# Optimization experiments

Hardware: AMD Instinct MI355X
Metric: run time of the kernel (lower is better)

## Reference

```python
import jax, jax.numpy as jnp
import numpy as np

TEMPERATURE = 0.07
N, D, NUM_CLASSES = 8192, 1024, 128


def setup_inputs() -> dict:
    key = jax.random.key(0)
    k1, k2 = jax.random.split(key)
    embeddings = jax.random.normal(k1, (N, D), dtype=jnp.float32)
    labels = jax.random.randint(k2, (N,), 0, NUM_CLASSES, dtype=jnp.int64)
    return {"embeddings": embeddings, "labels": labels}


def reference(embeddings, labels):
    # L2-normalize rows (eps matches F.normalize default clamp of 1e-12 on the norm)
    norm = jnp.maximum(jnp.linalg.norm(embeddings, axis=-1, keepdims=True), 1e-12)
    emb = embeddings / norm
    # [N, N] similarity scaled by temperature
    sim = jnp.matmul(emb, emb.T) / TEMPERATURE
    # positive mask: same label, diagonal zeroed
    pos_mask = (labels[:, None] == labels[None, :]).astype(sim.dtype)
    pos_mask = pos_mask * (1.0 - jnp.eye(sim.shape[0], dtype=sim.dtype))
    exp_sim = jnp.exp(sim)
    sum_exp = exp_sim.sum(axis=1)              # [N]
    pos_sum = (exp_sim * pos_mask).sum(axis=1)  # [N]
    loss = -jnp.log(pos_sum / sum_exp)
    return loss.mean()
```

## Files before the change

kernel.cpp:

```cpp
#include <hip/hip_runtime.h>
#include <hip/hip_bf16.h>
#include <math.h>

#define N 8192
#define D 1024
#define BM 256
#define BK 64
#define NTIL 32
#define NBLK 528
#define ITERS 8

typedef __bf16 bf16_t;
typedef bf16_t bf16x4 __attribute__((ext_vector_type(4)));
typedef bf16_t bf16x8 __attribute__((ext_vector_type(8)));
typedef float f32x4 __attribute__((ext_vector_type(4)));

__global__ __launch_bounds__(256) void norm_cast(const float* __restrict__ in,
                                                 bf16_t* __restrict__ out,
                                                 float* __restrict__ sumExp,
                                                 float* __restrict__ posSum) {
    const int wave = threadIdx.x >> 6, lane = threadIdx.x & 63;
    const int row  = blockIdx.x * 4 + wave;
    const float4* src = (const float4*)(in + (size_t)row * D);
    float4 v[4];
    float ss = 0.f;
    #pragma unroll
    for (int i = 0; i < 4; ++i) {
        v[i] = src[lane + 64 * i];
        ss += v[i].x * v[i].x + v[i].y * v[i].y + v[i].z * v[i].z + v[i].w * v[i].w;
    }
    #pragma unroll
    for (int off = 32; off >= 1; off >>= 1) ss += __shfl_xor(ss, off, 64);
    const float scale = 1.0f / fmaxf(sqrtf(ss), 1e-12f);
    bf16x4* dst = (bf16x4*)(out + (size_t)row * D);
    #pragma unroll
    for (int i = 0; i < 4; ++i) {
        bf16x4 o;
        o[0] = (bf16_t)(v[i].x * scale);
        o[1] = (bf16_t)(v[i].y * scale);
        o[2] = (bf16_t)(v[i].z * scale);
        o[3] = (bf16_t)(v[i].w * scale);
        dst[lane + 64 * i] = o;
    }
    if (lane == 0) { sumExp[row] = 0.f; posSum[row] = 0.f; }
}

__global__ __launch_bounds__(512, 2) void gemm_fused(const bf16_t* __restrict__ E,
                                                     const int* __restrict__ labels,
                                                     float* __restrict__ sumExp,
                                                     float* __restrict__ posSum) {
    __shared__ bf16_t As[2][2][128 * 64];
    __shared__ bf16_t Bs[2][2][128 * 64];

    const int b0 = blockIdx.x;
    const int b  = (b0 & 7) * (NBLK / 8) + (b0 >> 3);

    int ti = (int)((sqrtf(8.0f * (float)b + 1.0f) - 1.0f) * 0.5f);
    while ((ti + 1) * (ti + 2) / 2 <= b) ++ti;
    while (ti * (ti + 1) / 2 > b) --ti;
    const int tj = b - ti * (ti + 1) / 2;
    const bool isDiag = (ti == tj);

    const int tid  = threadIdx.x;
    const int wave = tid >> 6;
    const int lane = tid & 63;
    const int lr   = lane & 15;
    const int q    = lane >> 4;
    const int wm   = wave >> 2;
    const int wn   = wave & 3;
    const int rowStart = ti * BM;
    const int colStart = tj * BM;

    f32x4 acc[8][4];
    #pragma unroll
    for (int m = 0; m < 8; ++m)
        #pragma unroll
        for (int n = 0; n < 4; ++n) acc[m][n] = {0.f, 0.f, 0.f, 0.f};

    const int r0  = tid >> 3;
    const int lu0 = tid & 7;
    const char* gA = (const char*)(E + (size_t)rowStart * D) + (size_t)r0 * (D * 2) + lu0 * 16;
    const char* gB = (const char*)(E + (size_t)colStart * D) + (size_t)r0 * (D * 2) + lu0 * 16;

    #define STAGE_A(buf, h, kb) do {                                                     \
        const char* g0_ = gA + (size_t)(h) * (128 * 2048) + (kb);                        \
        char* l0_ = (char*)&As[buf][h][0] + wave * 1024;                                 \
        __builtin_amdgcn_global_load_lds((const __attribute__((address_space(1))) void*)g0_, \
            (__attribute__((address_space(3))) void*)l0_, 16, 0, 0);                     \
        __builtin_amdgcn_global_load_lds(                                                \
            (const __attribute__((address_space(1))) void*)(g0_ + 64 * 2048),            \
            (__attribute__((address_space(3))) void*)(l0_ + 8192), 16, 0, 0);            \
    } while (0)
    #define STAGE_B(buf, h, kb) do {                                                     \
        const char* g0_ = gB + (size_t)(h) * (128 * 2048) + (kb);                        \
        char* l0_ = (char*)&Bs[buf][h][0] + wave * 1024;                                 \
        __builtin_amdgcn_global_load_lds((const __attribute__((address_space(1))) void*)g0_, \
            (__attribute__((address_space(3))) void*)l0_, 16, 0, 0);                     \
        __builtin_amdgcn_global_load_lds(                                                \
            (const __attribute__((address_space(1))) void*)(g0_ + 64 * 2048),            \
            (__attribute__((address_space(3))) void*)(l0_ + 8192), 16, 0, 0);            \
    } while (0)

    const int su0 = (0 + q) * 16;
    const int su1 = (4 + q) * 16;
    const char* rA0 = (const char*)&As[0][wm][0] + lr * 128;
    const char* rA1 = (const char*)&As[1][wm][0] + lr * 128;
    const char* rB0 = (const char*)&Bs[0][wn >> 1][0] + (wn & 1) * 8192 + lr * 128;
    const char* rB1 = (const char*)&Bs[1][wn >> 1][0] + (wn & 1) * 8192 + lr * 128;

    #define LD_A4(DST, RBASE, MOFFB, SU) do {                                            \
        _Pragma("unroll")                                                                \
        for (int m_ = 0; m_ < 4; ++m_)                                                   \
            DST[m_] = *(const bf16x8*)((RBASE) + (MOFFB) + m_ * 2048 + (SU));            \
    } while (0)
    #define LD_B4(DST, RBASE, SU) do {                                                   \
        _Pragma("unroll")                                                                \
        for (int n_ = 0; n_ < 4; ++n_)                                                   \
            DST[n_] = *(const bf16x8*)((RBASE) + n_ * 2048 + (SU));                      \
    } while (0)
    #define MFMA_QUAD(AF, BF, MO) do {                                                   \
        _Pragma("unroll")                                                                \
        for (int m_ = 0; m_ < 4; ++m_) {                                                 \
            _Pragma("unroll")                                                            \
            for (int n_ = 0; n_ < 4; ++n_)                                               \
                acc[(MO) + m_][n_] = __builtin_amdgcn_mfma_f32_16x16x32_bf16(            \
                    AF[m_], BF[n_], acc[(MO) + m_][n_], 0, 0, 0);                        \
        }                                                                                \
    } while (0)
    #define PHASE_MID() do {                                                             \
        __builtin_amdgcn_s_barrier();                                                    \
        asm volatile("s_waitcnt lgkmcnt(0)");                                            \
        __builtin_amdgcn_sched_barrier(0);                                               \
        __builtin_amdgcn_s_setprio(1);                                                   \
    } while (0)
    #define PHASE_END() do {                                                             \
        __builtin_amdgcn_s_setprio(0);                                                   \
        __builtin_amdgcn_s_barrier();                                                    \
    } while (0)

    bf16x8 a0[4], a1[4], bq0[4], bq1[4];

    STAGE_B(0, 0, 0);  STAGE_B(0, 1, 0);
    STAGE_A(0, 0, 0);  STAGE_A(0, 1, 0);
    STAGE_B(1, 0, 128); STAGE_B(1, 1, 128);
    asm volatile("s_waitcnt vmcnt(4)" ::: "memory");
    __builtin_amdgcn_sched_barrier(0);
    __builtin_amdgcn_s_barrier();

    #pragma unroll 1
    for (int it = 0; it < ITERS; ++it) {
        const bool lastIt = (it == ITERS - 1);
        const int kb1 = (2 * it + 1) * 128;
        const int kb2 = (2 * it + 2) * 128;
        const int kb3 = (2 * it + 3) * 128;

        LD_A4(a0, rA0, 0, su0);
        LD_B4(bq0, rB0, su0);
        STAGE_A(1, 0, kb1);
        PHASE_MID();
        MFMA_QUAD(a0, bq0, 0);
        PHASE_END();

        LD_A4(a1, rA0, 0, su1);
        LD_B4(bq1, rB0, su1);
        STAGE_A(1, 1, kb1);
        PHASE_MID();
        MFMA_QUAD(a1, bq1, 0);
        PHASE_END();

        LD_A4(a0, rA0, 8192, su0);
        if (!lastIt) STAGE_B(0, 0, kb2);
        PHASE_MID();
        MFMA_QUAD(a0, bq0, 4);
        PHASE_END();

        LD_A4(a1, rA0, 8192, su1);
        if (!lastIt) {
            STAGE_B(0, 1, kb2);
            asm volatile("s_waitcnt vmcnt(4)" ::: "memory");
        } else {
            asm volatile("s_waitcnt vmcnt(0)" ::: "memory");
        }
        __builtin_amdgcn_sched_barrier(0);
        PHASE_MID();
        MFMA_QUAD(a1, bq1, 4);
        PHASE_END();

        LD_A4(a0, rA1, 0, su0);
        LD_B4(bq0, rB1, su0);
        if (!lastIt) STAGE_A(0, 0, kb2);
        PHASE_MID();
        MFMA_QUAD(a0, bq0, 0);
        PHASE_END();

        LD_A4(a1, rA1, 0, su1);
        LD_B4(bq1, rB1, su1);
        if (!lastIt) STAGE_A(0, 1, kb2);
        PHASE_MID();
        MFMA_QUAD(a1, bq1, 0);
        PHASE_END();

        LD_A4(a0, rA1, 8192, su0);
        if (!lastIt) STAGE_B(1, 0, kb3);
        PHASE_MID();
        MFMA_QUAD(a0, bq0, 4);
        PHASE_END();

        LD_A4(a1, rA1, 8192, su1);
        if (!lastIt) {
            STAGE_B(1, 1, kb3);
            asm volatile("s_waitcnt vmcnt(4)" ::: "memory");
            __builtin_amdgcn_sched_barrier(0);
        }
        PHASE_MID();
        MFMA_QUAD(a1, bq1, 4);
        PHASE_END();
    }

    const float invT = 1.0f / 0.07f;
    int lc[4];
    #pragma unroll
    for (int n = 0; n < 4; ++n)
        lc[n] = labels[colStart + wn * 64 + n * 16 + lr];

    float colAll[4] = {0.f, 0.f, 0.f, 0.f};
    float colPos[4] = {0.f, 0.f, 0.f, 0.f};
    #pragma unroll
    for (int m = 0; m < 8; ++m) {
        #pragma unroll
        for (int e = 0; e < 4; ++e) {
            const int rloc = wm * 128 + m * 16 + q * 4 + e;
            const int gi   = rowStart + rloc;
            const int li   = labels[gi];
            float s_all = 0.f, s_pos = 0.f;
            #pragma unroll
            for (int n = 0; n < 4; ++n) {
                const int cloc = wn * 64 + n * 16 + lr;
                const int gj   = colStart + cloc;
                const float v  = __expf(acc[m][n][e] * invT);
                const bool same = (lc[n] == li);
                s_all += v;
                if (same && gi != gj) s_pos += v;
                if (!isDiag) {
                    colAll[n] += v;
                    if (same) colPos[n] += v;
                }
            }
            #pragma unroll
            for (int off = 1; off < 16; off <<= 1) {
                s_all += __shfl_xor(s_all, off, 64);
                s_pos += __shfl_xor(s_pos, off, 64);
            }
            if (lr == 0) {
                atomicAdd(&sumExp[gi], s_all);
                atomicAdd(&posSum[gi], s_pos);
            }
        }
    }
    if (!isDiag) {
        #pragma unroll
        for (int n = 0; n < 4; ++n) {
            float a = colAll[n], p = colPos[n];
            a += __shfl_xor(a, 16, 64);  a += __shfl_xor(a, 32, 64);
            p += __shfl_xor(p, 16, 64);  p += __shfl_xor(p, 32, 64);
            if (q == 0) {
                const int gj = colStart + wn * 64 + n * 16 + lr;
                atomicAdd(&sumExp[gj], a);
                atomicAdd(&posSum[gj], p);
            }
        }
    }
}

__global__ __launch_bounds__(1024) void finalize(const float* __restrict__ sumExp,
                                                 const float* __restrict__ posSum,
                                                 float* __restrict__ out) {
    const int tid = threadIdx.x;
    float s = 0.f;
    #pragma unroll
    for (int i = tid; i < N; i += 1024)
        s += __logf(sumExp[i] / posSum[i]);
    #pragma unroll
    for (int off = 32; off >= 1; off >>= 1) s += __shfl_xor(s, off, 64);
    __shared__ float red[16];
    if ((tid & 63) == 0) red[tid >> 6] = s;
    __syncthreads();
    if (tid == 0) {
        float t = 0.f;
        #pragma unroll
        for (int i = 0; i < 16; ++i) t += red[i];
        out[0] = t / (float)N;
    }
}

extern "C" void kernel_launch(void* const* d_in, const int* in_sizes, int n_in,
                              void* d_out, int out_size, void* d_ws, size_t ws_size,
                              hipStream_t stream) {
    const float* emb    = (const float*)d_in[0];
    const int*   labels = (const int*)d_in[1];
    float* out = (float*)d_out;

    float*  sumExp = (float*)d_ws;
    float*  posSum = sumExp + N;
    bf16_t* EN     = (bf16_t*)((char*)d_ws + (size_t)2 * N * sizeof(float));

    norm_cast<<<N / 4, 256, 0, stream>>>(emb, EN, sumExp, posSum);

    gemm_fused<<<NBLK, 512, 0, stream>>>(EN, labels, sumExp, posSum);

    finalize<<<1, 1024, 0, stream>>>(sumExp, posSum, out);
}
```

Before: 239.9 us.

## Split last tile-row into quarter-tile blocks and XOR-swizzle LDS layout

The 16 tiles of the last 256-row tile band (ti=31) are split into 64 quarter-size 128x128 blocks with a separate simpler GEMM path, so total block count becomes 576 and the tail wave is better balanced across CUs. Separately, the global-to-LDS load column and LDS read offsets are XOR-swizzled by row to reduce LDS bank conflicts. The quarter path adds more atomic traffic and a less pipelined loop (waits vmcnt(0) each iteration).

```diff
diff --git a/kernel.cpp b/kernel.cpp
--- a/kernel.cpp
+++ b/kernel.cpp
@@ -6,8 +6,9 @@
 #define D 1024
 #define BM 256
 #define BK 64
-#define NTIL 32
-#define NBLK 528
+#define NQUART 64
+#define NFULL 512
+#define NBLK (NQUART + NFULL)
 #define ITERS 8
 
 typedef __bf16 bf16_t;
@@ -52,8 +53,150 @@
     __shared__ bf16_t As[2][2][128 * 64];
     __shared__ bf16_t Bs[2][2][128 * 64];
 
-    const int b0 = blockIdx.x;
-    const int b  = (b0 & 7) * (NBLK / 8) + (b0 >> 3);
+    const int tid  = threadIdx.x;
+    const int wave = tid >> 6;
+    const int lane = tid & 63;
+    const int lr   = lane & 15;
+    const int q    = lane >> 4;
+    const float invT = 1.0f / 0.07f;
+
+    const int su0 = ((0 + q) ^ (lane & 7)) * 16;
+    const int su1 = ((4 + q) ^ (lane & 7)) * 16;
+
+    #define PHASE_MID() do {                                                             \
+        __builtin_amdgcn_s_barrier();                                                    \
+        asm volatile("s_waitcnt lgkmcnt(0)");                                            \
+        __builtin_amdgcn_sched_barrier(0);                                               \
+        __builtin_amdgcn_s_setprio(1);                                                   \
+    } while (0)
+    #define PHASE_END() do {                                                             \
+        __builtin_amdgcn_s_setprio(0);                                                   \
+        __builtin_amdgcn_s_barrier();                                                    \
+    } while (0)
+
+    if (blockIdx.x < NQUART) {
+        const int qb = ((int)blockIdx.x & 7) * 8 + ((int)blockIdx.x >> 3);
+        const int p  = qb >> 2, qd = qb & 3;
+        const int rowStart = 31 * BM + (qd >> 1) * 128;
+        const int colStart = p * BM + (qd & 1) * 128;
+        const int wm2 = wave >> 2;
+        const int wn2 = wave & 3;
+
+        f32x4 acc[4][2];
+        #pragma unroll
+        for (int m = 0; m < 4; ++m) { acc[m][0] = {0,0,0,0}; acc[m][1] = {0,0,0,0}; }
+
+        const int r0  = tid >> 3;
+        const int lu0 = (tid & 7) ^ (r0 & 7);
+        const char* gA = (const char*)(E + (size_t)rowStart * D) + (size_t)r0 * (D * 2) + lu0 * 16;
+        const char* gB = (const char*)(E + (size_t)colStart * D) + (size_t)r0 * (D * 2) + lu0 * 16;
+
+        #define QSTAGE(buf, kb) do {                                                     \
+            const char* ga_ = gA + (kb);                                                 \
+            const char* gb_ = gB + (kb);                                                 \
+            char* la_ = (char*)&As[buf][0][0] + wave * 1024;                             \
+            char* lb_ = (char*)&Bs[buf][0][0] + wave * 1024;                             \
+            __builtin_amdgcn_global_load_lds((const __attribute__((address_space(1))) void*)ga_, \
+                (__attribute__((address_space(3))) void*)la_, 16, 0, 0);                 \
+            __builtin_amdgcn_global_load_lds(                                            \
+                (const __attribute__((address_space(1))) void*)(ga_ + 64 * 2048),        \
+                (__attribute__((address_space(3))) void*)(la_ + 8192), 16, 0, 0);        \
+            __builtin_amdgcn_global_load_lds((const __attribute__((address_space(1))) void*)gb_, \
+                (__attribute__((address_space(3))) void*)lb_, 16, 0, 0);                 \
+            __builtin_amdgcn_global_load_lds(                                            \
+                (const __attribute__((address_space(1))) void*)(gb_ + 64 * 2048),        \
+                (__attribute__((address_space(3))) void*)(lb_ + 8192), 16, 0, 0);        \
+        } while (0)
+
+        bf16x8 qa[4], qbf[2];
+        #define QLD(SU, BUF) do {                                                        \
+            const char* aB_ = (const char*)&As[BUF][0][0] + (wm2 * 64 + lr) * 128 + (SU);\
+            const char* bB_ = (const char*)&Bs[BUF][0][0] + (wn2 * 32 + lr) * 128 + (SU);\
+            _Pragma("unroll")                                                            \
+            for (int m_ = 0; m_ < 4; ++m_)                                               \
+                qa[m_] = *(const bf16x8*)(aB_ + m_ * 2048);                              \
+            qbf[0] = *(const bf16x8*)(bB_);                                              \
+            qbf[1] = *(const bf16x8*)(bB_ + 2048);                                       \
+        } while (0)
+        #define QMFMA() do {                                                             \
+            _Pragma("unroll")                                                            \
+            for (int m_ = 0; m_ < 4; ++m_) {                                             \
+                _Pragma("unroll")                                                        \
+                for (int n_ = 0; n_ < 2; ++n_)                                           \
+                    acc[m_][n_] = __builtin_amdgcn_mfma_f32_16x16x32_bf16(               \
+                        qa[m_], qbf[n_], acc[m_][n_], 0, 0, 0);                          \
+            }                                                                            \
+        } while (0)
+
+        QSTAGE(0, 0);
+        asm volatile("s_waitcnt vmcnt(0)" ::: "memory");
+        __builtin_amdgcn_sched_barrier(0);
+        __builtin_amdgcn_s_barrier();
+
+        #pragma unroll 1
+        for (int it = 0; it < 16; ++it) {
+            const int buf = it & 1;
+            QLD(su0, buf);
+            if (it < 15) QSTAGE(buf ^ 1, (it + 1) * 128);
+            PHASE_MID();
+            QMFMA();
+            PHASE_END();
+            QLD(su1, buf);
+            asm volatile("s_waitcnt vmcnt(0)" ::: "memory");
+            __builtin_amdgcn_sched_barrier(0);
+            PHASE_MID();
+            QMFMA();
+            PHASE_END();
+        }
+
+        int lc[2];
+        lc[0] = labels[colStart + wn2 * 32 + lr];
+        lc[1] = labels[colStart + wn2 * 32 + 16 + lr];
+        float colAll[2] = {0.f, 0.f}, colPos[2] = {0.f, 0.f};
+        #pragma unroll
+        for (int m = 0; m < 4; ++m) {
+            #pragma unroll
+            for (int e = 0; e < 4; ++e) {
+                const int gi = rowStart + wm2 * 64 + m * 16 + q * 4 + e;
+                const int li = labels[gi];
+                float s_all = 0.f, s_pos = 0.f;
+                #pragma unroll
+                for (int n = 0; n < 2; ++n) {
+                    const float v = __expf(acc[m][n][e] * invT);
+                    const bool same = (lc[n] == li);
+                    s_all += v;
+                    if (same) s_pos += v;
+                    colAll[n] += v;
+                    if (same) colPos[n] += v;
+                }
+                #pragma unroll
+                for (int off = 1; off < 16; off <<= 1) {
+                    s_all += __shfl_xor(s_all, off, 64);
+                    s_pos += __shfl_xor(s_pos, off, 64);
+                }
+                if (lr == 0) {
+                    atomicAdd(&sumExp[gi], s_all);
+                    atomicAdd(&posSum[gi], s_pos);
+                }
+            }
+        }
+        #pragma unroll
+        for (int n = 0; n < 2; ++n) {
+            float a = colAll[n], pp = colPos[n];
+            a += __shfl_xor(a, 16, 64);  a += __shfl_xor(a, 32, 64);
+            pp += __shfl_xor(pp, 16, 64); pp += __shfl_xor(pp, 32, 64);
+            if (q == 0) {
+                const int gj = colStart + wn2 * 32 + n * 16 + lr;
+                atomicAdd(&sumExp[gj], a);
+                atomicAdd(&posSum[gj], pp);
+            }
+        }
+        return;
+    }
+
+    const int f0 = (int)blockIdx.x - NQUART;
+    const int f  = (f0 & 7) * (NFULL / 8) + (f0 >> 3);
+    const int b  = (f < 496) ? f : f + 16;
 
     int ti = (int)((sqrtf(8.0f * (float)b + 1.0f) - 1.0f) * 0.5f);
     while ((ti + 1) * (ti + 2) / 2 <= b) ++ti;
@@ -61,11 +204,6 @@
     const int tj = b - ti * (ti + 1) / 2;
     const bool isDiag = (ti == tj);
 
-    const int tid  = threadIdx.x;
-    const int wave = tid >> 6;
-    const int lane = tid & 63;
-    const int lr   = lane & 15;
-    const int q    = lane >> 4;
     const int wm   = wave >> 2;
     const int wn   = wave & 3;
     const int rowStart = ti * BM;
@@ -78,7 +216,7 @@
         for (int n = 0; n < 4; ++n) acc[m][n] = {0.f, 0.f, 0.f, 0.f};
 
     const int r0  = tid >> 3;
-    const int lu0 = tid & 7;
+    const int lu0 = (tid & 7) ^ (r0 & 7);
     const char* gA = (const char*)(E + (size_t)rowStart * D) + (size_t)r0 * (D * 2) + lu0 * 16;
     const char* gB = (const char*)(E + (size_t)colStart * D) + (size_t)r0 * (D * 2) + lu0 * 16;
 
@@ -101,8 +239,6 @@
             (__attribute__((address_space(3))) void*)(l0_ + 8192), 16, 0, 0);            \
     } while (0)
 
-    const int su0 = (0 + q) * 16;
-    const int su1 = (4 + q) * 16;
     const char* rA0 = (const char*)&As[0][wm][0] + lr * 128;
     const char* rA1 = (const char*)&As[1][wm][0] + lr * 128;
     const char* rB0 = (const char*)&Bs[0][wn >> 1][0] + (wn & 1) * 8192 + lr * 128;
@@ -127,16 +263,6 @@
                     AF[m_], BF[n_], acc[(MO) + m_][n_], 0, 0, 0);                        \
         }                                                                                \
     } while (0)
-    #define PHASE_MID() do {                                                             \
-        __builtin_amdgcn_s_barrier();                                                    \
-        asm volatile("s_waitcnt lgkmcnt(0)");                                            \
-        __builtin_amdgcn_sched_barrier(0);                                               \
-        __builtin_amdgcn_s_setprio(1);                                                   \
-    } while (0)
-    #define PHASE_END() do {                                                             \
-        __builtin_amdgcn_s_setprio(0);                                                   \
-        __builtin_amdgcn_s_barrier();                                                    \
-    } while (0)
 
     bf16x8 a0[4], a1[4], bq0[4], bq1[4];
 
@@ -217,7 +343,6 @@
         PHASE_END();
     }
 
-    const float invT = 1.0f / 0.07f;
     int lc[4];
     #pragma unroll
     for (int n = 0; n < 4; ++n)
```

Result: faster. 206.7 us (-13.8%).
